# Optimization experiments

Hardware: AMD Instinct MI355X
Metric: run time of the kernel (lower is better)

## Reference

```python
import jax, jax.numpy as jnp
import numpy as np

HEAD_DIM = 64
N_HEADS = 25
N_KV_HEADS = 5
WINDOW = 1024
N_META = 128
EPS = 1e-6
ROPE_BASE = 10000.0


def _rmsnorm(x, w):
    # per-head RMSNorm over last dim, computed in fp32 (matches HymbaRMSNorm)
    xf = x.astype(jnp.float32)
    var = jnp.mean(xf * xf, axis=-1, keepdims=True)
    return w * (xf * jax.lax.rsqrt(var + EPS)).astype(x.dtype)


def _rotate_half(x):
    x1, x2 = jnp.split(x, 2, axis=-1)
    return jnp.concatenate((-x2, x1), axis=-1)


def _rope_cos_sin(position_ids):
    # equivalent to indexing the cached cos/sin tables with position_ids
    inv_freq = 1.0 / (ROPE_BASE ** (jnp.arange(0, HEAD_DIM, 2, dtype=jnp.float32) / HEAD_DIM))
    freqs = position_ids.astype(jnp.float32)[..., None] * inv_freq  # [B,T,hd/2]
    emb = jnp.concatenate((freqs, freqs), axis=-1)                   # [B,T,hd]
    return jnp.cos(emb)[:, None], jnp.sin(emb)[:, None]              # [B,1,T,hd]


def setup_inputs() -> dict:
    key = jax.random.key(0)
    k1, k2, k3, k4, k5 = jax.random.split(key, 5)
    B, T = 2, 2048
    return {
        "query_states": jax.random.normal(k1, (B, T, N_HEADS * HEAD_DIM), dtype=jnp.float32),
        "key_states": jax.random.normal(k2, (B, T, N_KV_HEADS * HEAD_DIM), dtype=jnp.float32),
        "value_states": jax.random.normal(k3, (B, T, N_KV_HEADS * HEAD_DIM), dtype=jnp.float32),
        "q_norm_w": jax.random.uniform(k4, (HEAD_DIM,), dtype=jnp.float32, minval=0.5, maxval=1.5),
        "k_norm_w": jax.random.uniform(k5, (HEAD_DIM,), dtype=jnp.float32, minval=0.5, maxval=1.5),
        "position_ids": jnp.broadcast_to(jnp.arange(T, dtype=jnp.int32), (B, T)),
    }


def reference(query_states, key_states, value_states, q_norm_w, k_norm_w, position_ids):
    B, T, _ = query_states.shape
    # [B, H, T, hd]
    q = query_states.reshape(B, T, N_HEADS, HEAD_DIM).transpose(0, 2, 1, 3)
    k = key_states.reshape(B, T, N_KV_HEADS, HEAD_DIM).transpose(0, 2, 1, 3)
    v = value_states.reshape(B, T, N_KV_HEADS, HEAD_DIM).transpose(0, 2, 1, 3)

    # per-head QK RMSNorm
    q = _rmsnorm(q, q_norm_w)
    k = _rmsnorm(k, k_norm_w)

    # RoPE
    cos, sin = _rope_cos_sin(position_ids)
    q = q * cos + _rotate_half(q) * sin
    k = k * cos + _rotate_half(k) * sin

    # GQA: repeat each kv head num_heads // num_kv_heads times (consecutively)
    n_rep = N_HEADS // N_KV_HEADS
    k_e = jnp.repeat(k, n_rep, axis=1)
    v_e = jnp.repeat(v, n_rep, axis=1)

    scale = 1.0 / np.sqrt(HEAD_DIM)
    scores = jnp.einsum("bhqd,bhkd->bhqk", q, k_e) * scale

    # SWA mask: causal AND (in sliding window OR meta/memory token)
    q_idx = jnp.arange(T)[:, None]
    k_idx = jnp.arange(T)[None, :]
    attend = (k_idx <= q_idx) & ((k_idx >= q_idx - WINDOW + 1) | (k_idx < N_META))
    scores = jnp.where(attend, scores, -jnp.inf)

    attn_weights = jax.nn.softmax(scores, axis=-1)
    out = jnp.einsum("bhqk,bhkd->bhqd", attn_weights, v_e)
    return out.transpose(0, 2, 1, 3).reshape(B, T, N_HEADS * HEAD_DIM)
```

## Files before the change

### kernel.cpp

```cpp
#include <hip/hip_runtime.h>
#include <cmath>

typedef float  f32x4  __attribute__((ext_vector_type(4)));
typedef __bf16 bf16x8 __attribute__((ext_vector_type(8)));
typedef unsigned int u32x4 __attribute__((ext_vector_type(4)));
typedef unsigned int u32x2 __attribute__((ext_vector_type(2)));
typedef unsigned int   u32;
typedef unsigned short u16;

#define HEAD_DIM 64
#define N_HEADS  25
#define N_KV     5
#define WINDOW   1024
#define N_META   128
#define B_       2
#define T_       2048
#define QB       64
#define NTILES   (T_ / 64)
#define TILE_U32 2048
#define SM_BIAS  (-20.0f)

static __device__ __forceinline__ u16 bf16_bits(float f) {
  __bf16 h = (__bf16)f;
  return __builtin_bit_cast(u16, h);
}
static __device__ __forceinline__ u32 pack2(float lo, float hi) {
  return ((u32)bf16_bits(hi) << 16) | bf16_bits(lo);
}
static __device__ __forceinline__ float fexp2(float x) {
  return __builtin_amdgcn_exp2f(x);
}
static __device__ __forceinline__ void gload16(const u32* g, u32* l) {
  __builtin_amdgcn_global_load_lds((const __attribute__((address_space(1))) u32*)g,
                                   (__attribute__((address_space(3))) u32*)l, 16, 0, 0);
}

__global__ __launch_bounds__(256) void prep_kernel(
    const float* __restrict__ k_in, const float* __restrict__ k_w,
    const float* __restrict__ v_in, const int* __restrict__ pos_ids,
    u32* __restrict__ k_ws, u32* __restrict__ v_ws)
{
  const int blk = blockIdx.x;
  const int tid = threadIdx.x;

  if (blk < B_ * N_KV * NTILES) {
    int tile = blk & (NTILES - 1);
    int bk   = blk >> 5;
    int kvh  = bk % N_KV, b = bk / N_KV;
    int t0   = tile * 64;

    __shared__ u16 Tl[64][72];

    #pragma unroll
    for (int it = 0; it < 4; ++it) {
      int idx = it * 256 + tid;
      int kl = idx >> 4, dq = idx & 15;
      const float4 f = *(const float4*)&v_in[((size_t)(b * T_ + t0 + kl)) * (N_KV * HEAD_DIM) + kvh * HEAD_DIM + dq * 4];
      Tl[dq * 4 + 0][kl] = bf16_bits(f.x);
      Tl[dq * 4 + 1][kl] = bf16_bits(f.y);
      Tl[dq * 4 + 2][kl] = bf16_bits(f.z);
      Tl[dq * 4 + 3][kl] = bf16_bits(f.w);
    }
    __syncthreads();

    u32* outb = v_ws + (size_t)blk * TILE_U32;
    #pragma unroll
    for (int it = 0; it < 8; ++it) {
      int o = it * 256 + tid;
      int d = o >> 5, c = o & 31;
      u32 w = ((u32)Tl[d][2 * c + 1] << 16) | Tl[d][2 * c];
      int a = c >> 4, bs = (c >> 3) & 1, gp = (c >> 1) & 3, e = c & 1;
      int sp = (4 * a + gp) ^ (d & 7);
      outb[d * 32 + sp * 4 + 2 * bs + e] = w;
    }
    return;
  }

  int gw   = (((blk - B_ * N_KV * NTILES) * 256 + tid) >> 6);
  int lane = tid & 63;
  if (gw >= B_ * T_ * N_KV) return;
  int kvh = gw % N_KV;
  int bt  = gw / N_KV;

  float x = k_in[(size_t)bt * (N_KV * HEAD_DIM) + kvh * HEAD_DIM + lane];
  float ss = x * x;
  #pragma unroll
  for (int off = 32; off; off >>= 1) ss += __shfl_xor(ss, off);
  float y = k_w[lane] * x * rsqrtf(ss * (1.f / 64.f) + 1e-6f);

  int   pos = pos_ids[bt];
  float ang = (float)pos * powf(10000.f, -(float)(lane & 31) * (1.f / 32.f));
  float c, s;
  sincosf(ang, &s, &c);
  float part = __shfl_xor(y, 32);
  float r = (lane < 32) ? (y * c - part * s) : (y * c + part * s);

  u16 mybits = bf16_bits(r);
  u32 pb = (u32)(u16)__shfl_xor((int)mybits, 1);
  u32 w  = (pb << 16) | mybits;
  int b = bt / T_, t = bt % T_;
  if (!(lane & 1)) {
    int c32 = lane >> 1;
    int kl = t & 63, tile = t >> 6;
    int sp = (c32 >> 2) ^ (kl & 7);
    k_ws[(((size_t)(b * N_KV + kvh) * NTILES + tile)) * TILE_U32 + kl * 32 + sp * 4 + (c32 & 3)] = w;
  }
}

__global__ __launch_bounds__(256, 4) void attn_kernel(
    const float* __restrict__ q_in, const float* __restrict__ q_w,
    const int* __restrict__ pos_ids,
    const u32* __restrict__ kws, const u32* __restrict__ vws,
    float* __restrict__ out)
{
  const int i  = blockIdx.x;
  const int x  = i & 7, k = i >> 3;
  const int gA = (5 * x) >> 2;
  const int a0 = 200 * x - 160 * gA;
  const int nB = 40 + a0;
  int grp, j_;
  if (k < nB) { grp = gA + 1; j_ = k; }
  else        { grp = gA;     j_ = a0 + (k - nB); }
  const int qt  = 31 - j_ / 5;
  const int hh  = j_ % 5;
  const int b   = grp / 5;
  const int kvh = grp % 5;
  const int h   = kvh * 5 + hh;
  const int qb  = qt * QB;
  const int tid = threadIdx.x, wid = tid >> 6, lane = tid & 63;
  const int l15 = lane & 15, g = lane >> 4;
  const int qrow0 = wid * 16;

  __shared__ u32 Ks[2 * TILE_U32];
  __shared__ u32 Vt[2 * TILE_U32];

  const int nt    = (qt <= 18) ? (qt + 1) : 19;
  const int shift = qt - 18;

  const size_t kvbase = ((size_t)(b * N_KV + kvh)) * NTILES * TILE_U32;
  const u32* kb = kws + kvbase;
  const u32* vb = vws + kvbase;

  #pragma unroll
  for (int j = 0; j < 4; ++j) {
    int ci = (wid << 2) | j;
    if (ci < 8) gload16(kb + ci * 256 + lane * 4, &Ks[ci * 256]);
    else        gload16(vb + (ci - 8) * 256 + lane * 4, &Vt[(ci - 8) * 256]);
  }

  {
    const int   jbase = (4 * l15) & 31;
    const float r32   = 0.74989420933f;
    float fr[4];
    fr[0] = powf(10000.f, -(float)jbase * (1.f / 32.f));
    fr[1] = fr[0] * r32; fr[2] = fr[1] * r32; fr[3] = fr[2] * r32;

    const int t0g = b * T_ + qb + qrow0;
    int pos_prev = pos_ids[t0g + g];
    float cc[4], sn[4], c4[4], s4[4];
    #pragma unroll
    for (int e = 0; e < 4; ++e) {
      sincosf((float)pos_prev * fr[e], &sn[e], &cc[e]);
      sincosf(4.f * fr[e], &s4[e], &c4[e]);
    }
    const float4 wv = *(const float4*)&q_w[4 * l15];
    #pragma unroll
    for (int it = 0; it < 4; ++it) {
      const int row = 4 * it + g;
      if (it) {
        int pos = pos_ids[t0g + row];
        if (__all(pos == pos_prev + 4)) {
          #pragma unroll
          for (int e = 0; e < 4; ++e) {
            float c2 = cc[e] * c4[e] - sn[e] * s4[e];
            sn[e] = sn[e] * c4[e] + cc[e] * s4[e];
            cc[e] = c2;
          }
        } else {
          #pragma unroll
          for (int e = 0; e < 4; ++e) sincosf((float)pos * fr[e], &sn[e], &cc[e]);
        }
        pos_prev = pos;
      }
      const float4 xv = *(const float4*)&q_in[((size_t)(t0g + row)) * (N_HEADS * HEAD_DIM) + h * HEAD_DIM + 4 * l15];
      float ss = xv.x * xv.x + xv.y * xv.y + xv.z * xv.z + xv.w * xv.w;
      ss += __shfl_xor(ss, 1); ss += __shfl_xor(ss, 2);
      ss += __shfl_xor(ss, 4); ss += __shfl_xor(ss, 8);
      const float rn = rsqrtf(ss * (1.f / 64.f) + 1e-6f);
      float y[4] = {wv.x * xv.x * rn, wv.y * xv.y * rn, wv.z * xv.z * rn, wv.w * xv.w * rn};
      float rv[4];
      #pragma unroll
      for (int e = 0; e < 4; ++e) {
        float part = __shfl_xor(y[e], 8);
        rv[e] = ((l15 < 8) ? (y[e] * cc[e] - part * sn[e])
                           : (y[e] * cc[e] + part * sn[e])) * 0.18033688f;
      }
      u32x2 w2;
      w2.x = pack2(rv[0], rv[1]);
      w2.y = pack2(rv[2], rv[3]);
      *(u32x2*)&Ks[TILE_U32 + (qrow0 + row) * 32 + 2 * l15] = w2;
    }
  }
  __syncthreads();

  bf16x8 qf[2];
  #pragma unroll
  for (int ks = 0; ks < 2; ++ks)
    qf[ks] = *(const bf16x8*)&Ks[TILE_U32 + (qrow0 + l15) * 32 + 16 * ks + 4 * g];
  __syncthreads();

  float l_part = 0.f;
  f32x4 acc_o[4];
  #pragma unroll
  for (int mt = 0; mt < 4; ++mt) acc_o[mt] = (f32x4)(0.f);

  const int q_abs = qb + qrow0 + l15;

  int buf = 0;
  for (int i2 = 0; i2 < nt; ++i2) {
    if (i2 + 1 < nt) {
      int tn = (qt <= 18 || i2 + 1 < 2) ? (i2 + 1) : (i2 + 1 + shift);
      const u32* kt = kb + (size_t)tn * TILE_U32;
      const u32* vt = vb + (size_t)tn * TILE_U32;
      u32* kd = &Ks[(buf ^ 1) * TILE_U32];
      u32* vd = &Vt[(buf ^ 1) * TILE_U32];
      #pragma unroll
      for (int j = 0; j < 4; ++j) {
        int ci = (wid << 2) | j;
        if (ci < 8) gload16(kt + ci * 256 + lane * 4, kd + ci * 256);
        else        gload16(vt + (ci - 8) * 256 + lane * 4, vd + (ci - 8) * 256);
      }
    }
    const int k0 = ((qt <= 18 || i2 < 2) ? i2 : i2 + shift) << 6;

    f32x4 accs[4];
    #pragma unroll
    for (int mt = 0; mt < 4; ++mt) accs[mt] = (f32x4)(SM_BIAS);
    #pragma unroll
    for (int ks = 0; ks < 2; ++ks) {
      #pragma unroll
      for (int mt = 0; mt < 4; ++mt) {
        bf16x8 kf = *(const bf16x8*)&Ks[buf * TILE_U32 + (16 * mt + l15) * 32 + (((4 * ks + g) ^ (l15 & 7)) << 2)];
        accs[mt] = __builtin_amdgcn_mfma_f32_16x16x32_bf16(kf, qf[ks], accs[mt], 0, 0, 0);
      }
    }

    const bool do_mask = (i2 == nt - 1) || (qt >= 18 && i2 == 2);
    if (do_mask) {
      #pragma unroll
      for (int mt = 0; mt < 4; ++mt)
        #pragma unroll
        for (int rg = 0; rg < 4; ++rg) {
          int key = k0 + 16 * mt + 4 * g + rg;
          bool ok = (key <= q_abs) && ((key >= q_abs - (WINDOW - 1)) || (key < N_META));
          accs[mt][rg] = ok ? accs[mt][rg] : -INFINITY;
        }
    }
    float rsum = 0.f;
    #pragma unroll
    for (int mt = 0; mt < 4; ++mt)
      #pragma unroll
      for (int rg = 0; rg < 4; ++rg) {
        float pi = fexp2(accs[mt][rg]);
        accs[mt][rg] = pi;
        rsum += pi;
      }
    l_part += rsum;

    #pragma unroll
    for (int ks2 = 0; ks2 < 2; ++ks2) {
      const int m0 = 2 * ks2, m1 = 2 * ks2 + 1;
      u32x4 aw;
      aw.x = pack2(accs[m0][0], accs[m0][1]);
      aw.y = pack2(accs[m0][2], accs[m0][3]);
      aw.z = pack2(accs[m1][0], accs[m1][1]);
      aw.w = pack2(accs[m1][2], accs[m1][3]);
      bf16x8 af = __builtin_bit_cast(bf16x8, aw);
      #pragma unroll
      for (int mt2 = 0; mt2 < 4; ++mt2) {
        bf16x8 vf = *(const bf16x8*)&Vt[buf * TILE_U32 + (16 * mt2 + l15) * 32 + (((4 * ks2 + g) ^ (l15 & 7)) << 2)];
        acc_o[mt2] = __builtin_amdgcn_mfma_f32_16x16x32_bf16(af, vf, acc_o[mt2], 0, 0, 0);
      }
    }

    __syncthreads();
    buf ^= 1;
  }

  float lsum = l_part;
  lsum += __shfl_xor(lsum, 16);
  lsum += __shfl_xor(lsum, 32);
  float l4[4];
  #pragma unroll
  for (int rg = 0; rg < 4; ++rg) l4[rg] = __shfl(lsum, 4 * g + rg);
  #pragma unroll
  for (int mt2 = 0; mt2 < 4; ++mt2)
    #pragma unroll
    for (int rg = 0; rg < 4; ++rg) {
      int t = qb + qrow0 + 4 * g + rg;
      out[((size_t)(b * T_ + t)) * (N_HEADS * HEAD_DIM) + h * HEAD_DIM + 16 * mt2 + l15] =
          acc_o[mt2][rg] / l4[rg];
    }
}

extern "C" void kernel_launch(void* const* d_in, const int* in_sizes, int n_in,
                              void* d_out, int out_size, void* d_ws, size_t ws_size,
                              hipStream_t stream) {
  const float* q   = (const float*)d_in[0];
  const float* k   = (const float*)d_in[1];
  const float* v   = (const float*)d_in[2];
  const float* qw  = (const float*)d_in[3];
  const float* kw  = (const float*)d_in[4];
  const int*   pos = (const int*)d_in[5];

  u32* kp = (u32*)d_ws;
  u32* vp = kp + (size_t)B_ * N_KV * NTILES * TILE_U32;
  float* outp = (float*)d_out;

  prep_kernel<<<B_ * N_KV * NTILES + 5120, 256, 0, stream>>>(k, kw, v, pos, kp, vp);
  attn_kernel<<<1600, 256, 0, stream>>>(q, qw, pos, kp, vp, outp);
}
```

Before: 58.23 us.

## Halve KV tile to 32 keys to double occupancy in attention loop

Shrinks each K/V tile processed per iteration from 64 to 32 keys, halving shared memory per block and raising the launch-bounds occupancy hint from 4 to 8 blocks per CU. V tiles are gathered from the 64-key workspace layout with a remapped swizzle, and Q staging is split across the K and V buffers. The intent is to hide memory latency with more resident waves. The cost is twice as many loop iterations and barriers, with less MFMA work per sync.

```diff
diff --git a/kernel.cpp b/kernel.cpp
--- a/kernel.cpp
+++ b/kernel.cpp
@@ -18,6 +18,7 @@
 #define QB       64
 #define NTILES   (T_ / 64)
 #define TILE_U32 2048
+#define T32_U32  1024
 #define SM_BIAS  (-20.0f)
 
 static __device__ __forceinline__ u16 bf16_bits(float f) {
@@ -107,7 +108,7 @@
   }
 }
 
-__global__ __launch_bounds__(256, 4) void attn_kernel(
+__global__ __launch_bounds__(256, 8) void attn_kernel(
     const float* __restrict__ q_in, const float* __restrict__ q_w,
     const int* __restrict__ pos_ids,
     const u32* __restrict__ kws, const u32* __restrict__ vws,
@@ -131,21 +132,27 @@
   const int l15 = lane & 15, g = lane >> 4;
   const int qrow0 = wid * 16;
 
-  __shared__ u32 Ks[2 * TILE_U32];
-  __shared__ u32 Vt[2 * TILE_U32];
-
-  const int nt    = (qt <= 18) ? (qt + 1) : 19;
-  const int shift = qt - 18;
+  __shared__ u32 Ks[2 * T32_U32];
+  __shared__ u32 Vt[2 * T32_U32];
+
+  const int nt      = (qt <= 17) ? (2 * qt + 2) : 38;
+  const int shift32 = 2 * qt - 36;
 
   const size_t kvbase = ((size_t)(b * N_KV + kvh)) * NTILES * TILE_U32;
   const u32* kb = kws + kvbase;
   const u32* vb = vws + kvbase;
 
   #pragma unroll
-  for (int j = 0; j < 4; ++j) {
-    int ci = (wid << 2) | j;
-    if (ci < 8) gload16(kb + ci * 256 + lane * 4, &Ks[ci * 256]);
-    else        gload16(vb + (ci - 8) * 256 + lane * 4, &Vt[(ci - 8) * 256]);
+  for (int j = 0; j < 2; ++j) {
+    int ci = (wid << 1) | j;
+    if (ci < 4) {
+      gload16(kb + ci * 256 + lane * 4, &Ks[ci * 256]);
+    } else {
+      int c = ci - 4;
+      int d = c * 16 + (lane >> 2), p = lane & 3;
+      int hd = (d >> 2) & 1;
+      gload16(vb + d * 32 + hd * 16 + p * 4, &Vt[c * 256]);
+    }
   }
 
   {
@@ -154,6 +161,9 @@
     float fr[4];
     fr[0] = powf(10000.f, -(float)jbase * (1.f / 32.f));
     fr[1] = fr[0] * r32; fr[2] = fr[1] * r32; fr[3] = fr[2] * r32;
+
+    u32* qstage = ((wid < 2) ? Ks : Vt) + T32_U32;
+    const int rbase = (qrow0 & 31);
 
     const int t0g = b * T_ + qb + qrow0;
     int pos_prev = pos_ids[t0g + g];
@@ -198,15 +208,19 @@
       u32x2 w2;
       w2.x = pack2(rv[0], rv[1]);
       w2.y = pack2(rv[2], rv[3]);
-      *(u32x2*)&Ks[TILE_U32 + (qrow0 + row) * 32 + 2 * l15] = w2;
+      *(u32x2*)&qstage[(rbase + row) * 32 + 2 * l15] = w2;
     }
   }
   __syncthreads();
 
   bf16x8 qf[2];
-  #pragma unroll
-  for (int ks = 0; ks < 2; ++ks)
-    qf[ks] = *(const bf16x8*)&Ks[TILE_U32 + (qrow0 + l15) * 32 + 16 * ks + 4 * g];
+  {
+    const u32* qstage = ((wid < 2) ? Ks : Vt) + T32_U32;
+    const int rbase = (qrow0 & 31);
+    #pragma unroll
+    for (int ks = 0; ks < 2; ++ks)
+      qf[ks] = *(const bf16x8*)&qstage[(rbase + l15) * 32 + 16 * ks + 4 * g];
+  }
   __syncthreads();
 
   float l_part = 0.f;
@@ -219,36 +233,40 @@
   int buf = 0;
   for (int i2 = 0; i2 < nt; ++i2) {
     if (i2 + 1 < nt) {
-      int tn = (qt <= 18 || i2 + 1 < 2) ? (i2 + 1) : (i2 + 1 + shift);
-      const u32* kt = kb + (size_t)tn * TILE_U32;
-      const u32* vt = vb + (size_t)tn * TILE_U32;
-      u32* kd = &Ks[(buf ^ 1) * TILE_U32];
-      u32* vd = &Vt[(buf ^ 1) * TILE_U32];
-      #pragma unroll
-      for (int j = 0; j < 4; ++j) {
-        int ci = (wid << 2) | j;
-        if (ci < 8) gload16(kt + ci * 256 + lane * 4, kd + ci * 256);
-        else        gload16(vt + (ci - 8) * 256 + lane * 4, vd + (ci - 8) * 256);
-      }
-    }
-    const int k0 = ((qt <= 18 || i2 < 2) ? i2 : i2 + shift) << 6;
-
-    f32x4 accs[4];
-    #pragma unroll
-    for (int mt = 0; mt < 4; ++mt) accs[mt] = (f32x4)(SM_BIAS);
+      int tn = (qt <= 17 || i2 + 1 < 4) ? (i2 + 1) : (i2 + 1 + shift32);
+      u32* kd = &Ks[(buf ^ 1) * T32_U32];
+      u32* vd = &Vt[(buf ^ 1) * T32_U32];
+      #pragma unroll
+      for (int j = 0; j < 2; ++j) {
+        int ci = (wid << 1) | j;
+        if (ci < 4) {
+          gload16(kb + (size_t)tn * T32_U32 + ci * 256 + lane * 4, kd + ci * 256);
+        } else {
+          int c = ci - 4;
+          int d = c * 16 + (lane >> 2), p = lane & 3;
+          int hd = (tn & 1) ^ ((d >> 2) & 1);
+          gload16(vb + (size_t)(tn >> 1) * TILE_U32 + d * 32 + hd * 16 + p * 4, vd + c * 256);
+        }
+      }
+    }
+    const int k0 = ((qt <= 17 || i2 < 4) ? i2 : i2 + shift32) << 5;
+
+    f32x4 accs[2];
+    accs[0] = (f32x4)(SM_BIAS);
+    accs[1] = (f32x4)(SM_BIAS);
     #pragma unroll
     for (int ks = 0; ks < 2; ++ks) {
       #pragma unroll
-      for (int mt = 0; mt < 4; ++mt) {
-        bf16x8 kf = *(const bf16x8*)&Ks[buf * TILE_U32 + (16 * mt + l15) * 32 + (((4 * ks + g) ^ (l15 & 7)) << 2)];
+      for (int mt = 0; mt < 2; ++mt) {
+        bf16x8 kf = *(const bf16x8*)&Ks[buf * T32_U32 + (16 * mt + l15) * 32 + (((4 * ks + g) ^ (l15 & 7)) << 2)];
         accs[mt] = __builtin_amdgcn_mfma_f32_16x16x32_bf16(kf, qf[ks], accs[mt], 0, 0, 0);
       }
     }
 
-    const bool do_mask = (i2 == nt - 1) || (qt >= 18 && i2 == 2);
+    const bool do_mask = (i2 >= nt - 2) || (qt >= 18 && (i2 == 4 || i2 == 5));
     if (do_mask) {
       #pragma unroll
-      for (int mt = 0; mt < 4; ++mt)
+      for (int mt = 0; mt < 2; ++mt)
         #pragma unroll
         for (int rg = 0; rg < 4; ++rg) {
           int key = k0 + 16 * mt + 4 * g + rg;
@@ -258,7 +276,7 @@
     }
     float rsum = 0.f;
     #pragma unroll
-    for (int mt = 0; mt < 4; ++mt)
+    for (int mt = 0; mt < 2; ++mt)
       #pragma unroll
       for (int rg = 0; rg < 4; ++rg) {
         float pi = fexp2(accs[mt][rg]);
@@ -267,18 +285,16 @@
       }
     l_part += rsum;
 
-    #pragma unroll
-    for (int ks2 = 0; ks2 < 2; ++ks2) {
-      const int m0 = 2 * ks2, m1 = 2 * ks2 + 1;
+    {
       u32x4 aw;
-      aw.x = pack2(accs[m0][0], accs[m0][1]);
-      aw.y = pack2(accs[m0][2], accs[m0][3]);
-      aw.z = pack2(accs[m1][0], accs[m1][1]);
-      aw.w = pack2(accs[m1][2], accs[m1][3]);
+      aw.x = pack2(accs[0][0], accs[0][1]);
+      aw.y = pack2(accs[0][2], accs[0][3]);
+      aw.z = pack2(accs[1][0], accs[1][1]);
+      aw.w = pack2(accs[1][2], accs[1][3]);
       bf16x8 af = __builtin_bit_cast(bf16x8, aw);
       #pragma unroll
       for (int mt2 = 0; mt2 < 4; ++mt2) {
-        bf16x8 vf = *(const bf16x8*)&Vt[buf * TILE_U32 + (16 * mt2 + l15) * 32 + (((4 * ks2 + g) ^ (l15 & 7)) << 2)];
+        bf16x8 vf = *(const bf16x8*)&Vt[buf * T32_U32 + (16 * mt2 + l15) * 16 + ((g ^ (l15 & 3)) << 2)];
         acc_o[mt2] = __builtin_amdgcn_mfma_f32_16x16x32_bf16(af, vf, acc_o[mt2], 0, 0, 0);
       }
     }
```

Result: slower. 84.95 us (+45.9%).
